# Optimization experiments

Measured on AMD Instinct MI355X. Metric: run time of the kernel, lower is better.

## Reference

```python
import jax, jax.numpy as jnp
import numpy as np

B, T, D, H, E, K, F = 8, 1024, 512, 8, 8, 2, 2048
HD = D // H
EPS = 1e-5


def _layernorm(x, g, b):
    m = jnp.mean(x, axis=-1, keepdims=True)
    v = jnp.mean((x - m) ** 2, axis=-1, keepdims=True)
    return (x - m) * jax.lax.rsqrt(v + EPS) * g + b


def setup_inputs() -> dict:
    key = jax.random.key(0)
    ks = jax.random.split(key, 12)
    s = lambda d: 1.0 / np.sqrt(d)
    return {
        "x": jax.random.normal(ks[0], (B, T, D), jnp.float32),
        "ln1_g": jnp.ones((D,), jnp.float32),
        "ln1_b": jnp.zeros((D,), jnp.float32),
        "ln2_g": jnp.ones((D,), jnp.float32),
        "ln2_b": jnp.zeros((D,), jnp.float32),
        "Wqkv": jax.random.normal(ks[1], (D, 3 * D), jnp.float32) * s(D),
        "bqkv": jnp.zeros((3 * D,), jnp.float32),
        "Wo": jax.random.normal(ks[2], (D, D), jnp.float32) * s(D),
        "bo": jnp.zeros((D,), jnp.float32),
        "Wg": jax.random.normal(ks[3], (D, E), jnp.float32) * s(D),
        "We1": jax.random.normal(ks[4], (E, D, F), jnp.float32) * s(D),
        "be1": jnp.zeros((E, F), jnp.float32),
        "We2": jax.random.normal(ks[5], (E, F, D), jnp.float32) * s(F),
        "be2": jnp.zeros((E, D), jnp.float32),
    }


def _attn(x, Wqkv, bqkv, Wo, bo):
    qkv = x @ Wqkv + bqkv                      # [B,T,3D]
    q, k, v = jnp.split(qkv, 3, axis=-1)
    q = q.reshape(B, T, H, HD)
    k = k.reshape(B, T, H, HD)
    v = v.reshape(B, T, H, HD)
    scores = jnp.einsum("bqhd,bkhd->bhqk", q, k) / np.sqrt(HD)
    causal = jnp.tril(jnp.ones((T, T), bool))
    scores = jnp.where(causal, scores, jnp.finfo(scores.dtype).min)
    p = jax.nn.softmax(scores, axis=-1)
    o = jnp.einsum("bhqk,bkhd->bqhd", p, v).reshape(B, T, D)
    return o @ Wo + bo


def _moe(h, Wg, We1, be1, We2, be2):
    hf = h.reshape(-1, D)                      # [N,D]
    N = hf.shape[0]
    probs = jax.nn.softmax(hf @ Wg, axis=-1)   # [N,E]
    topw, topi = jax.lax.top_k(probs, K)       # [N,K]
    topw = topw / jnp.sum(topw, axis=-1, keepdims=True)
    gates = jnp.zeros((N, E), hf.dtype).at[jnp.arange(N)[:, None], topi].add(topw)
    out = jnp.zeros_like(hf)
    for e in range(E):                         # fixed small expert loop
        hid = jax.nn.gelu(hf @ We1[e] + be1[e])
        out = out + gates[:, e:e + 1] * (hid @ We2[e] + be2[e])
    return out.reshape(h.shape)


def reference(x, ln1_g, ln1_b, ln2_g, ln2_b, Wqkv, bqkv, Wo, bo, Wg, We1, be1, We2, be2):
    # Pipeline chunking over batch is a scheduling detail; math is the plain block.
    h = x + _attn(_layernorm(x, ln1_g, ln1_b), Wqkv, bqkv, Wo, bo)
    return h + _moe(_layernorm(h, ln2_g, ln2_b), Wg, We1, be1, We2, be2)
```

## Files before the change

kernel.cpp:

```cpp
#include <hip/hip_runtime.h>


typedef unsigned short u16;
typedef unsigned int   u32;
typedef unsigned long long u64;
typedef __attribute__((ext_vector_type(8))) short short8;
typedef __attribute__((ext_vector_type(4))) float f32x4;

#define DEV static __device__ __forceinline__

DEV u16 f2bf(float f){
  union { float f; u32 u; } x; x.f = f;
  return (u16)((x.u + 0x7FFFu + ((x.u >> 16) & 1u)) >> 16);
}
DEV float bf2f(u16 b){
  union { u32 u; float f; } x; x.u = ((u32)b) << 16; return x.f;
}
DEV f32x4 mfma16(short8 a, short8 b, f32x4 c){
  return __builtin_amdgcn_mfma_f32_16x16x32_bf16(a, b, c, 0, 0, 0);
}
DEV void g2l16(const void* g, void* l){
  __builtin_amdgcn_global_load_lds((const __attribute__((address_space(1))) u32*)g,
                                   (__attribute__((address_space(3))) u32*)l, 16, 0, 0);
}
DEV void wait_vm0(){ asm volatile("s_waitcnt vmcnt(0)" ::: "memory"); }

__global__ __launch_bounds__(256) void transpose_cvt2(const float* __restrict__ src,
    u16* __restrict__ dh, u16* __restrict__ dl, int R, int C)
{
  __shared__ float tile[32][33];
  const size_t zb = (size_t)blockIdx.z * R * C;
  src += zb; dh += zb; dl += zb;
  const int tx = threadIdx.x, ty = threadIdx.y;
  const int c0 = blockIdx.x * 32, r0 = blockIdx.y * 32;
  #pragma unroll
  for (int i = 0; i < 4; ++i)
    tile[ty + i*8][tx] = src[(size_t)(r0 + ty + i*8) * C + c0 + tx];
  __syncthreads();
  #pragma unroll
  for (int i = 0; i < 4; ++i){
    float v = tile[tx][ty + i*8];
    size_t o = (size_t)(c0 + ty + i*8) * R + r0 + tx;
    u16 hb = f2bf(v);
    dh[o] = hb;
    dl[o] = f2bf(v - bf2f(hb));
  }
}

__global__ __launch_bounds__(256) void transpose_cvt1(const float* __restrict__ src,
    u16* __restrict__ d, int R, int C)
{
  __shared__ float tile[32][33];
  const size_t zb = (size_t)blockIdx.z * R * C;
  src += zb; d += zb;
  const int tx = threadIdx.x, ty = threadIdx.y;
  const int c0 = blockIdx.x * 32, r0 = blockIdx.y * 32;
  #pragma unroll
  for (int i = 0; i < 4; ++i)
    tile[ty + i*8][tx] = src[(size_t)(r0 + ty + i*8) * C + c0 + tx];
  __syncthreads();
  #pragma unroll
  for (int i = 0; i < 4; ++i)
    d[(size_t)(c0 + ty + i*8) * R + r0 + tx] = f2bf(tile[tx][ty + i*8]);
}

__global__ __launch_bounds__(256) void ln1_kernel(const float* __restrict__ x,
    const float* __restrict__ g, const float* __restrict__ b,
    u16* __restrict__ yh, u16* __restrict__ yl)
{
  const int wid = threadIdx.x >> 6, lane = threadIdx.x & 63;
  const int row = blockIdx.x * 4 + wid;
  const float* xr = x + (size_t)row * 512 + lane * 8;
  f32x4 t0 = ((const f32x4*)xr)[0], t1 = ((const f32x4*)xr)[1];
  float v[8];
  #pragma unroll
  for (int j = 0; j < 8; ++j) v[j] = (j < 4) ? t0[j] : t1[j-4];
  float s = 0.f, q = 0.f;
  #pragma unroll
  for (int j = 0; j < 8; ++j){ s += v[j]; q += v[j]*v[j]; }
  #pragma unroll
  for (int o = 32; o; o >>= 1){ s += __shfl_xor(s, o); q += __shfl_xor(q, o); }
  const float mean = s * (1.f/512.f);
  const float var  = q * (1.f/512.f) - mean*mean;
  const float rstd = rsqrtf(var + 1e-5f);
  f32x4 g0 = ((const f32x4*)(g + lane*8))[0], g1 = ((const f32x4*)(g + lane*8))[1];
  f32x4 b0 = ((const f32x4*)(b + lane*8))[0], b1 = ((const f32x4*)(b + lane*8))[1];
  short8 vh, vl;
  #pragma unroll
  for (int j = 0; j < 8; ++j){
    float gg = (j < 4) ? g0[j] : g1[j-4];
    float bb = (j < 4) ? b0[j] : b1[j-4];
    float y = (v[j]-mean)*rstd*gg + bb;
    u16 hb = f2bf(y);
    vh[j] = (short)hb;
    vl[j] = (short)f2bf(y - bf2f(hb));
  }
  ((short8*)(yh + (size_t)row*512 + lane*8))[0] = vh;
  ((short8*)(yl + (size_t)row*512 + lane*8))[0] = vl;
}

template<int MODE>
__global__ __launch_bounds__(256) void gemm_split2(
    const u16* __restrict__ Ah, const u16* __restrict__ Al,
    const u16* __restrict__ Bh, const u16* __restrict__ Bl,
    const float* __restrict__ bias, int K,
    u16* __restrict__ q_h, u16* __restrict__ q_l, u16* __restrict__ q_m,
    u16* __restrict__ k_h, u16* __restrict__ k_l, u16* __restrict__ k_m,
    u16* __restrict__ v_h, u16* __restrict__ v_l,
    const float* __restrict__ xres, float* __restrict__ hout)
{
  __shared__ u16 Ash[2][128*32], Asl[2][128*32], Bsh[2][128*32], Bsl[2][128*32];
  const int tid = threadIdx.x;
  const int wid = tid >> 6, lane = tid & 63;
  const int wr = wid >> 1, wc = wid & 1;
  const int lr = lane & 15, lg = lane >> 4;
  const int m0 = blockIdx.x * 128, n0 = blockIdx.y * 128;

  size_t aoff[2], boff[2];
  u32 ldso[2];
  #pragma unroll
  for (int r = 0; r < 2; ++r){
    int i = r*256 + tid;
    int row = i >> 2, cc = i & 3;
    int scc = cc ^ ((row >> 1) & 3);
    aoff[r] = ((size_t)(m0+row)*K + scc*8) * 2;
    boff[r] = ((size_t)(n0+row)*K + scc*8) * 2;
    ldso[r] = (u32)(r*256 + wid*64) * 8;
  }

  f32x4 acc[4][4];
  #pragma unroll
  for (int a = 0; a < 4; ++a)
    #pragma unroll
    for (int b = 0; b < 4; ++b) acc[a][b] = 0;

  const char* pAh = (const char*)Ah; const char* pAl = (const char*)Al;
  const char* pBh = (const char*)Bh; const char* pBl = (const char*)Bl;

  auto stage = [&](int sb, int ks){
    const size_t kb = (size_t)ks * 64;
    #pragma unroll
    for (int r = 0; r < 2; ++r){
      g2l16(pAh + aoff[r] + kb, &Ash[sb][0] + ldso[r]);
      g2l16(pAl + aoff[r] + kb, &Asl[sb][0] + ldso[r]);
      g2l16(pBh + boff[r] + kb, &Bsh[sb][0] + ldso[r]);
      g2l16(pBl + boff[r] + kb, &Bsl[sb][0] + ldso[r]);
    }
  };

  const int nks = K >> 5;
  stage(0, 0);
  wait_vm0();
  __syncthreads();
  int buf = 0;
  for (int ks = 0; ks < nks; ++ks){
    if (ks + 1 < nks) stage(buf ^ 1, ks + 1);
    short8 ah[4], al[4], bh[4], bl[4];
    #pragma unroll
    for (int mt = 0; mt < 4; ++mt){
      int row = wr*64 + mt*16 + lr;
      int kcs = lg ^ ((row >> 1) & 3);
      int o = row*32 + kcs*8;
      ah[mt] = *(const short8*)(&Ash[buf][0] + o);
      al[mt] = *(const short8*)(&Asl[buf][0] + o);
    }
    #pragma unroll
    for (int nt = 0; nt < 4; ++nt){
      int row = wc*64 + nt*16 + lr;
      int kcs = lg ^ ((row >> 1) & 3);
      int o = row*32 + kcs*8;
      bh[nt] = *(const short8*)(&Bsh[buf][0] + o);
      bl[nt] = *(const short8*)(&Bsl[buf][0] + o);
    }
    __builtin_amdgcn_s_setprio(1);
    #pragma unroll
    for (int mt = 0; mt < 4; ++mt)
      #pragma unroll
      for (int nt = 0; nt < 4; ++nt){
        f32x4 c = acc[mt][nt];
        c = mfma16(ah[mt], bh[nt], c);
        c = mfma16(ah[mt], bl[nt], c);
        c = mfma16(al[mt], bh[nt], c);
        acc[mt][nt] = c;
      }
    __builtin_amdgcn_s_setprio(0);
    wait_vm0();
    __syncthreads();
    buf ^= 1;
  }

  #pragma unroll
  for (int mt = 0; mt < 4; ++mt){
    #pragma unroll
    for (int nt = 0; nt < 4; ++nt){
      const int col = n0 + wc*64 + nt*16 + lr;
      const float bv = bias[col];
      #pragma unroll
      for (int r2 = 0; r2 < 4; ++r2){
        const int row = m0 + wr*64 + mt*16 + 4*lg + r2;
        const float val = acc[mt][nt][r2] + bv;
        if constexpr (MODE == 0){
          const int which = col >> 9, rem = col & 511;
          const int hh = rem >> 6, hd = rem & 63;
          const int b_ = row >> 10, t_ = row & 1023;
          const size_t idx = ((size_t)(b_*8 + hh)*1024 + t_)*64 + hd;
          const u16 hb = f2bf(val);
          if (which == 2){
            v_h[idx] = hb;
            v_l[idx] = f2bf(val - bf2f(hb));
          } else {
            const float r1 = val - bf2f(hb);
            const u16 lb = f2bf(r1);
            const u16 mb = f2bf(r1 - bf2f(lb));
            if (which == 0){ q_h[idx]=hb; q_l[idx]=lb; q_m[idx]=mb; }
            else           { k_h[idx]=hb; k_l[idx]=lb; k_m[idx]=mb; }
          }
        } else {
          const size_t o = (size_t)row*512 + col;
          hout[o] = val + xres[o];
        }
      }
    }
  }
}

__global__ __launch_bounds__(256) void attn_kernel(
    const u16* __restrict__ q_h, const u16* __restrict__ q_l, const u16* __restrict__ q_m,
    const u16* __restrict__ k_h, const u16* __restrict__ k_l, const u16* __restrict__ k_m,
    const u16* __restrict__ v_h, const u16* __restrict__ v_l,
    u16* __restrict__ aoh, u16* __restrict__ aol)
{
  __shared__ u16 Ksh[64*64], Ksl[64*64], Ksm[64*64];
  __shared__ u16 Vth[64*72], Vtl[64*72];
  __shared__ u16 Ph[4*16*72], Pl[4*16*72];
  const int tid = threadIdx.x, wid = tid >> 6, lane = tid & 63;
  const int lr = lane & 15, lg = lane >> 4;
  const int bfl = blockIdx.x;
  const int xcd = bfl & 7, jj_ = bfl >> 3;
  const int bh = xcd * 8 + (jj_ & 7);
  const int qt = 15 - (jj_ >> 3);
  const int q0 = qt * 64;
  const size_t base = (size_t)bh * 1024 * 64;

  short8 qfh[2], qfl[2], qfm[2];
  {
    const int qrow = q0 + wid*16 + lr;
    #pragma unroll
    for (int c = 0; c < 2; ++c){
      const size_t o = base + (size_t)qrow*64 + c*32 + lg*8;
      qfh[c] = *(const short8*)(q_h + o);
      qfl[c] = *(const short8*)(q_l + o);
      qfm[c] = *(const short8*)(q_m + o);
    }
  }
  f32x4 oacc[4];
  float m_r[4], l_r[4];
  #pragma unroll
  for (int nt = 0; nt < 4; ++nt) oacc[nt] = 0;
  #pragma unroll
  for (int r = 0; r < 4; ++r){ m_r[r] = -1e30f; l_r[r] = 0.f; }

  short8 kreg[3][2];
  short8 vreg[2][2];
  const int pp = tid & 31, d0 = (tid >> 5) * 8;

  auto load_tile = [&](int kt){
    #pragma unroll
    for (int r = 0; r < 2; ++r){
      const int i = r*256 + tid;
      const int row = i >> 3, cc = i & 7;
      const int scc = cc ^ (row & 7);
      const size_t go = base + (size_t)(kt*64 + row)*64 + scc*8;
      kreg[0][r] = *(const short8*)(k_h + go);
      kreg[1][r] = *(const short8*)(k_l + go);
      kreg[2][r] = *(const short8*)(k_m + go);
    }
    const size_t g0 = base + (size_t)(kt*64 + 2*pp)*64 + d0;
    vreg[0][0] = *(const short8*)(v_h + g0);
    vreg[0][1] = *(const short8*)(v_h + g0 + 64);
    vreg[1][0] = *(const short8*)(v_l + g0);
    vreg[1][1] = *(const short8*)(v_l + g0 + 64);
  };

  load_tile(0);
  for (int kt = 0; kt <= qt; ++kt){
    if (kt) __syncthreads();
    #pragma unroll
    for (int r = 0; r < 2; ++r){
      const int o = (r*256 + tid) * 8;
      *(short8*)(Ksh + o) = kreg[0][r];
      *(short8*)(Ksl + o) = kreg[1][r];
      *(short8*)(Ksm + o) = kreg[2][r];
    }
    #pragma unroll
    for (int j = 0; j < 8; ++j){
      u32 ph_ = (u32)(u16)vreg[0][0][j] | ((u32)(u16)vreg[0][1][j] << 16);
      u32 pl_ = (u32)(u16)vreg[1][0][j] | ((u32)(u16)vreg[1][1][j] << 16);
      *(u32*)(Vth + (d0+j)*72 + 2*pp) = ph_;
      *(u32*)(Vtl + (d0+j)*72 + 2*pp) = pl_;
    }
    __syncthreads();
    if (kt < qt) load_tile(kt + 1);
    __builtin_amdgcn_sched_barrier(0);

    f32x4 s[4];
    #pragma unroll
    for (int nt = 0; nt < 4; ++nt) s[nt] = 0;
    __builtin_amdgcn_s_setprio(1);
    #pragma unroll
    for (int c = 0; c < 2; ++c){
      #pragma unroll
      for (int nt = 0; nt < 4; ++nt){
        const int row = nt*16 + lr;
        const int kcs = (c*4 + lg) ^ (row & 7);
        const int o = row*64 + kcs*8;
        short8 kh_ = *(const short8*)(Ksh + o);
        short8 kl_ = *(const short8*)(Ksl + o);
        short8 km_ = *(const short8*)(Ksm + o);
        f32x4 cacc = s[nt];
        cacc = mfma16(qfh[c], kh_, cacc);
        cacc = mfma16(qfh[c], kl_, cacc);
        cacc = mfma16(qfl[c], kh_, cacc);
        cacc = mfma16(qfh[c], km_, cacc);
        cacc = mfma16(qfm[c], kh_, cacc);
        cacc = mfma16(qfl[c], kl_, cacc);
        s[nt] = cacc;
      }
    }
    __builtin_amdgcn_s_setprio(0);
    float sc[4][4];
    const bool last = (kt == qt);
    #pragma unroll
    for (int nt = 0; nt < 4; ++nt)
      #pragma unroll
      for (int r = 0; r < 4; ++r){
        float v = s[nt][r] * 0.125f;
        if (last){
          int qa = q0 + wid*16 + 4*lg + r;
          int ka = kt*64 + nt*16 + lr;
          if (ka > qa) v = -1e30f;
        }
        sc[nt][r] = v;
      }
    float pr[4][4];
    #pragma unroll
    for (int r = 0; r < 4; ++r){
      float mx = fmaxf(fmaxf(sc[0][r], sc[1][r]), fmaxf(sc[2][r], sc[3][r]));
      #pragma unroll
      for (int o2 = 8; o2; o2 >>= 1) mx = fmaxf(mx, __shfl_xor(mx, o2));
      const float nm = fmaxf(m_r[r], mx);
      const float al = __expf(m_r[r] - nm);
      float sum = 0.f;
      #pragma unroll
      for (int nt = 0; nt < 4; ++nt){
        float e_ = __expf(sc[nt][r] - nm);
        pr[nt][r] = e_;
        sum += e_;
      }
      #pragma unroll
      for (int o2 = 8; o2; o2 >>= 1) sum += __shfl_xor(sum, o2);
      l_r[r] = l_r[r]*al + sum;
      m_r[r] = nm;
      #pragma unroll
      for (int nt = 0; nt < 4; ++nt) oacc[nt][r] *= al;
    }
    #pragma unroll
    for (int nt = 0; nt < 4; ++nt)
      #pragma unroll
      for (int r = 0; r < 4; ++r){
        const float pv = pr[nt][r];
        const u16 hb = f2bf(pv);
        const u16 lb = f2bf(pv - bf2f(hb));
        const int o = wid*1152 + (4*lg + r)*72 + nt*16 + lr;
        Ph[o] = hb; Pl[o] = lb;
      }
    #pragma unroll
    for (int c = 0; c < 2; ++c){
      const int po = wid*1152 + lr*72 + c*32 + lg*8;
      short8 pah = *(const short8*)(Ph + po);
      short8 pal = *(const short8*)(Pl + po);
      __builtin_amdgcn_s_setprio(1);
      #pragma unroll
      for (int nt = 0; nt < 4; ++nt){
        const int vo = (nt*16 + lr)*72 + c*32 + lg*8;
        short8 vhf = *(const short8*)(Vth + vo);
        short8 vlf = *(const short8*)(Vtl + vo);
        f32x4 cacc = oacc[nt];
        cacc = mfma16(pah, vhf, cacc);
        cacc = mfma16(pah, vlf, cacc);
        cacc = mfma16(pal, vhf, cacc);
        oacc[nt] = cacc;
      }
      __builtin_amdgcn_s_setprio(0);
    }
  }

  const int b_ = bh >> 3, h_ = bh & 7;
  #pragma unroll
  for (int nt = 0; nt < 4; ++nt)
    #pragma unroll
    for (int r = 0; r < 4; ++r){
      const int qa = q0 + wid*16 + 4*lg + r;
      const float val = oacc[nt][r] / l_r[r];
      const size_t o = ((size_t)(b_*1024 + qa))*512 + h_*64 + nt*16 + lr;
      const u16 hb = f2bf(val);
      aoh[o] = hb;
      aol[o] = f2bf(val - bf2f(hb));
    }
}

__global__ __launch_bounds__(256) void ln2_gate_kernel(const float* __restrict__ h,
    const float* __restrict__ g, const float* __restrict__ b,
    const float* __restrict__ Wg, u16* __restrict__ y2,
    int* __restrict__ ge, float* __restrict__ gw)
{
  const int wid = threadIdx.x >> 6, lane = threadIdx.x & 63;
  const int row = blockIdx.x * 4 + wid;
  const float* xr = h + (size_t)row * 512 + lane * 8;
  f32x4 t0 = ((const f32x4*)xr)[0], t1 = ((const f32x4*)xr)[1];
  float v[8];
  #pragma unroll
  for (int j = 0; j < 8; ++j) v[j] = (j < 4) ? t0[j] : t1[j-4];
  float s = 0.f, q = 0.f;
  #pragma unroll
  for (int j = 0; j < 8; ++j){ s += v[j]; q += v[j]*v[j]; }
  #pragma unroll
  for (int o = 32; o; o >>= 1){ s += __shfl_xor(s, o); q += __shfl_xor(q, o); }
  const float mean = s * (1.f/512.f);
  const float var  = q * (1.f/512.f) - mean*mean;
  const float rstd = rsqrtf(var + 1e-5f);
  f32x4 g0 = ((const f32x4*)(g + lane*8))[0], g1 = ((const f32x4*)(g + lane*8))[1];
  f32x4 b0 = ((const f32x4*)(b + lane*8))[0], b1 = ((const f32x4*)(b + lane*8))[1];
  float yv[8];
  short8 yb;
  #pragma unroll
  for (int j = 0; j < 8; ++j){
    float gg = (j < 4) ? g0[j] : g1[j-4];
    float bb = (j < 4) ? b0[j] : b1[j-4];
    yv[j] = (v[j]-mean)*rstd*gg + bb;
    yb[j] = (short)f2bf(yv[j]);
  }
  ((short8*)(y2 + (size_t)row*512 + lane*8))[0] = yb;

  float lgt[8];
  #pragma unroll
  for (int e = 0; e < 8; ++e) lgt[e] = 0.f;
  #pragma unroll
  for (int j = 0; j < 8; ++j){
    const float* wr_ = Wg + (size_t)(lane*8 + j) * 8;
    #pragma unroll
    for (int e = 0; e < 8; ++e) lgt[e] += yv[j] * wr_[e];
  }
  #pragma unroll
  for (int o = 32; o; o >>= 1){
    #pragma unroll
    for (int e = 0; e < 8; ++e) lgt[e] += __shfl_xor(lgt[e], o);
  }
  if (lane == 0){
    int e0 = 0; float l0 = lgt[0];
    #pragma unroll
    for (int e = 1; e < 8; ++e) if (lgt[e] > l0){ l0 = lgt[e]; e0 = e; }
    int e1 = -1; float l1 = -3e38f;
    #pragma unroll
    for (int e = 0; e < 8; ++e) if (e != e0 && lgt[e] > l1){ l1 = lgt[e]; e1 = e; }
    const float t = expf(l1 - l0);
    const float w0 = 1.f / (1.f + t);
    const float w1 = t * w0;
    ge[row*2]   = e0; ge[row*2+1] = e1;
    gw[row*2]   = w0; gw[row*2+1] = w1;
  }
}

__global__ __launch_bounds__(256) void count_kernel(const int* __restrict__ ge,
                                                    int* __restrict__ cnt)
{
  const int i = blockIdx.x * 256 + threadIdx.x;
  const int lane = threadIdx.x & 63;
  const int e = ge[i];
  #pragma unroll
  for (int ex = 0; ex < 8; ++ex){
    u64 m = __ballot(e == ex);
    if (m && lane == (int)(__ffsll((long long)m) - 1))
      atomicAdd(&cnt[ex], __popcll(m));
  }
}

__global__ void offsets_kernel(int* cnt){
  if (threadIdx.x == 0){
    int o = 0, tp = 0;
    for (int e = 0; e < 8; ++e){
      cnt[8+e] = o; cnt[17+e] = o;
      cnt[25+e] = tp;
      o  += cnt[e];
      tp += (cnt[e] + 127) >> 7;
    }
    cnt[16] = o;
    cnt[33] = tp;
  }
}

__global__ __launch_bounds__(256) void scatter_kernel(const int* __restrict__ ge,
    const float* __restrict__ gw, int* __restrict__ cnt,
    int* __restrict__ rdst, float* __restrict__ rw)
{
  const int i = blockIdx.x * 256 + threadIdx.x;
  const int lane = threadIdx.x & 63;
  const int e = ge[i];
  const float w = gw[i];
  const u64 below = ((u64)1 << lane) - 1;
  int pos = -1;
  #pragma unroll
  for (int ex = 0; ex < 8; ++ex){
    u64 m = __ballot(e == ex);
    if (m){
      const int leader = (int)(__ffsll((long long)m) - 1);
      int base = 0;
      if (lane == leader) base = atomicAdd(&cnt[17 + ex], __popcll(m));
      base = __shfl(base, leader);
      if (e == ex) pos = base + __popcll(m & below);
    }
  }
  rdst[pos] = i;
  rw[pos]   = w;
}

template<int MODE, int TN, int BAND_M, int BPX>
__global__ __launch_bounds__(256, 4) void gemm_moe(
    const u16* __restrict__ A, const u16* __restrict__ Bt,
    const float* __restrict__ bias, int N, int K,
    const int* __restrict__ cntblk,
    const int* __restrict__ rdst, const float* __restrict__ rw,
    u16* __restrict__ hid, float* __restrict__ contrib)
{
  __shared__ u16 As[2][128*32], Bs[2][128*32];
  const int fid = blockIdx.x;
  const int xcd = fid & 7;
  const int j   = fid >> 3;
  const int bpb = BAND_M * TN;
  const int bi  = j / bpb;
  const int r_  = j % bpb;
  const int nt_ = r_ / BAND_M;
  const int mi  = r_ % BAND_M;
  const int mt  = (bi * 8 + xcd) * BAND_M + mi;
  if (mt >= cntblk[33]) return;
  int e = 7;
  #pragma unroll
  for (int k = 7; k >= 1; --k) if (mt < cntblk[25 + k]) e = k - 1;
  const int ce = cntblk[e];
  const int eo = cntblk[8 + e];
  const int m0 = (mt - cntblk[25 + e]) * 128;
  const int n0 = nt_ * 128;

  const int tid = threadIdx.x;
  const int wid = tid >> 6, lane = tid & 63;
  const int wr = wid >> 1, wc = wid & 1;
  const int lr = lane & 15, lg = lane >> 4;

  size_t aoff[2], boff[2];
  u32 ldso[2];
  #pragma unroll
  for (int r = 0; r < 2; ++r){
    int i = r*256 + tid;
    int row = i >> 2, cc = i & 3;
    int scc = cc ^ ((row >> 1) & 3);
    int p = eo + m0 + row;
    const int pmax = eo + ce - 1;
    if (p > pmax) p = pmax;
    const int arow = (MODE == 2) ? (rdst[p] >> 1) : p;
    aoff[r] = ((size_t)arow * K + scc*8) * 2;
    boff[r] = (((size_t)e * N + n0 + row) * K + scc*8) * 2;
    ldso[r] = (u32)(r*256 + wid*64) * 8;
  }

  f32x4 acc[4][4];
  #pragma unroll
  for (int a = 0; a < 4; ++a)
    #pragma unroll
    for (int b = 0; b < 4; ++b) acc[a][b] = 0;

  const char* pA = (const char*)A;
  const char* pB = (const char*)Bt;

  auto stage = [&](int sb, int ks){
    const size_t kb = (size_t)ks * 64;
    #pragma unroll
    for (int r = 0; r < 2; ++r){
      g2l16(pA + aoff[r] + kb, &As[sb][0] + ldso[r]);
      g2l16(pB + boff[r] + kb, &Bs[sb][0] + ldso[r]);
    }
  };

  const int nks = K >> 5;
  stage(0, 0);
  wait_vm0();
  __syncthreads();
  int buf = 0;
  for (int ks = 0; ks < nks; ++ks){
    if (ks + 1 < nks) stage(buf ^ 1, ks + 1);
    short8 av[4], bv[4];
    #pragma unroll
    for (int mt2 = 0; mt2 < 4; ++mt2){
      int row = wr*64 + mt2*16 + lr;
      int kcs = lg ^ ((row >> 1) & 3);
      av[mt2] = *(const short8*)(&As[buf][0] + row*32 + kcs*8);
    }
    #pragma unroll
    for (int nt2 = 0; nt2 < 4; ++nt2){
      int row = wc*64 + nt2*16 + lr;
      int kcs = lg ^ ((row >> 1) & 3);
      bv[nt2] = *(const short8*)(&Bs[buf][0] + row*32 + kcs*8);
    }
    __builtin_amdgcn_s_setprio(1);
    #pragma unroll
    for (int mt2 = 0; mt2 < 4; ++mt2)
      #pragma unroll
      for (int nt2 = 0; nt2 < 4; ++nt2)
        acc[mt2][nt2] = mfma16(av[mt2], bv[nt2], acc[mt2][nt2]);
    __builtin_amdgcn_s_setprio(0);
    wait_vm0();
    __syncthreads();
    buf ^= 1;
  }

  const float* bp = bias + (size_t)e * N;
  #pragma unroll
  for (int mt2 = 0; mt2 < 4; ++mt2){
    #pragma unroll
    for (int nt2 = 0; nt2 < 4; ++nt2){
      const int col = n0 + wc*64 + nt2*16 + lr;
      const float bv2 = bp[col];
      #pragma unroll
      for (int r2 = 0; r2 < 4; ++r2){
        const int lrow = wr*64 + mt2*16 + 4*lg + r2;
        if (m0 + lrow < ce){
          const int p = eo + m0 + lrow;
          const float val = acc[mt2][nt2][r2] + bv2;
          if constexpr (MODE == 2){
            const float gx = val;
            const float z2 = 1.5957691216057308f * (gx + 0.044715f*gx*gx*gx);
            const float gl = gx / (1.f + __expf(-z2));
            hid[(size_t)p * N + col] = f2bf(gl);
          } else {
            contrib[(size_t)rdst[p] * N + col] = val * rw[p];
          }
        }
      }
    }
  }
}

__global__ __launch_bounds__(256) void final_kernel(const float* __restrict__ h,
    const float* __restrict__ contrib, float* __restrict__ out)
{
  const int i = blockIdx.x * 256 + threadIdx.x;
  const int row = i >> 7, rem = i & 127;
  const f32x4* c4 = (const f32x4*)contrib;
  f32x4 hv = ((const f32x4*)h)[i];
  f32x4 a = c4[(size_t)(row*2) * 128 + rem];
  f32x4 b = c4[(size_t)(row*2) * 128 + 128 + rem];
  ((f32x4*)out)[i] = hv + a + b;
}

extern "C" void kernel_launch(void* const* d_in, const int* in_sizes, int n_in,
                              void* d_out, int out_size, void* d_ws, size_t ws_size,
                              hipStream_t stream)
{
  (void)in_sizes; (void)n_in; (void)out_size; (void)ws_size;
  const float* x    = (const float*)d_in[0];
  const float* ln1g = (const float*)d_in[1];
  const float* ln1b = (const float*)d_in[2];
  const float* ln2g = (const float*)d_in[3];
  const float* ln2b = (const float*)d_in[4];
  const float* Wqkv = (const float*)d_in[5];
  const float* bqkv = (const float*)d_in[6];
  const float* Wo   = (const float*)d_in[7];
  const float* bo   = (const float*)d_in[8];
  const float* Wg   = (const float*)d_in[9];
  const float* We1  = (const float*)d_in[10];
  const float* be1  = (const float*)d_in[11];
  const float* We2  = (const float*)d_in[12];
  const float* be2  = (const float*)d_in[13];
  float* out = (float*)d_out;

  char* ws = (char*)d_ws;
  size_t off_ = 0;
  auto alloc = [&](size_t bytes)->char*{
    char* p = ws + off_;
    off_ = (off_ + bytes + 255) & ~(size_t)255;
    return p;
  };
  u16* wqkvTh = (u16*)alloc((size_t)1536*512*2);
  u16* wqkvTl = (u16*)alloc((size_t)1536*512*2);
  u16* woTh   = (u16*)alloc((size_t)512*512*2);
  u16* woTl   = (u16*)alloc((size_t)512*512*2);
  u16* we1T   = (u16*)alloc((size_t)8*2048*512*2);
  u16* we2T   = (u16*)alloc((size_t)8*512*2048*2);
  u16* y1h    = (u16*)alloc((size_t)8192*512*2);
  u16* y1l    = (u16*)alloc((size_t)8192*512*2);
  u16* qh_    = (u16*)alloc((size_t)8192*64*8*2);
  u16* ql_    = (u16*)alloc((size_t)8192*64*8*2);
  u16* qm_    = (u16*)alloc((size_t)8192*64*8*2);
  u16* kh_    = (u16*)alloc((size_t)8192*64*8*2);
  u16* kl_    = (u16*)alloc((size_t)8192*64*8*2);
  u16* km_    = (u16*)alloc((size_t)8192*64*8*2);
  u16* vh_    = (u16*)alloc((size_t)8192*64*8*2);
  u16* vl_    = (u16*)alloc((size_t)8192*64*8*2);
  u16* aoh    = (u16*)alloc((size_t)8192*512*2);
  u16* aol    = (u16*)alloc((size_t)8192*512*2);
  float* hbuf = (float*)alloc((size_t)8192*512*4);
  u16* y2     = (u16*)alloc((size_t)8192*512*2);
  int* ge     = (int*)alloc((size_t)8192*2*4);
  float* gw   = (float*)alloc((size_t)8192*2*4);
  int* cnt    = (int*)alloc(256);
  int* rdst   = (int*)alloc((size_t)16384*4);
  float* rw   = (float*)alloc((size_t)16384*4);
  u16* hid    = (u16*)alloc((size_t)16384*2048*2);
  float* contrib = (float*)alloc((size_t)16384*512*4);

  (void)hipMemsetAsync(cnt, 0, 256, stream);

  const dim3 tb(32, 8);
  transpose_cvt2<<<dim3(48, 16, 1), tb, 0, stream>>>(Wqkv, wqkvTh, wqkvTl, 512, 1536);
  transpose_cvt2<<<dim3(16, 16, 1), tb, 0, stream>>>(Wo,   woTh,   woTl,   512, 512);
  transpose_cvt1<<<dim3(64, 16, 8), tb, 0, stream>>>(We1, we1T, 512, 2048);
  transpose_cvt1<<<dim3(16, 64, 8), tb, 0, stream>>>(We2, we2T, 2048, 512);

  ln1_kernel<<<2048, 256, 0, stream>>>(x, ln1g, ln1b, y1h, y1l);

  gemm_split2<0><<<dim3(64, 12), 256, 0, stream>>>(
      y1h, y1l, wqkvTh, wqkvTl, bqkv, 512,
      qh_, ql_, qm_, kh_, kl_, km_, vh_, vl_, nullptr, nullptr);

  attn_kernel<<<dim3(1024), 256, 0, stream>>>(
      qh_, ql_, qm_, kh_, kl_, km_, vh_, vl_, aoh, aol);

  gemm_split2<1><<<dim3(64, 4), 256, 0, stream>>>(
      aoh, aol, woTh, woTl, bo, 512,
      nullptr, nullptr, nullptr, nullptr, nullptr, nullptr, nullptr, nullptr,
      x, hbuf);

  ln2_gate_kernel<<<2048, 256, 0, stream>>>(hbuf, ln2g, ln2b, Wg, y2, ge, gw);
  count_kernel<<<64, 256, 0, stream>>>(ge, cnt);
  offsets_kernel<<<1, 64, 0, stream>>>(cnt);
  scatter_kernel<<<64, 256, 0, stream>>>(ge, gw, cnt, rdst, rw);

  gemm_moe<2, 16, 2, 9><<<dim3(2304), 256, 0, stream>>>(
      y2, we1T, be1, 2048, 512, cnt, rdst, rw, hid, nullptr);
  gemm_moe<3, 4, 2, 9><<<dim3(576), 256, 0, stream>>>(
      hid, we2T, be2, 512, 2048, cnt, rdst, rw, nullptr, contrib);

  final_kernel<<<4096, 256, 0, stream>>>(hbuf, contrib, out);
}
```

Measured before the change: 421.9 us.

## Split-K the MoE down-projection and atomically accumulate into output

```diff
diff --git a/kernel.cpp b/kernel.cpp
--- a/kernel.cpp
+++ b/kernel.cpp
@@ -412,12 +412,14 @@
 __global__ __launch_bounds__(256) void ln2_gate_kernel(const float* __restrict__ h,
     const float* __restrict__ g, const float* __restrict__ b,
     const float* __restrict__ Wg, u16* __restrict__ y2,
-    int* __restrict__ ge, float* __restrict__ gw)
+    int* __restrict__ ge, float* __restrict__ gw, float* __restrict__ outw)
 {
   const int wid = threadIdx.x >> 6, lane = threadIdx.x & 63;
   const int row = blockIdx.x * 4 + wid;
   const float* xr = h + (size_t)row * 512 + lane * 8;
   f32x4 t0 = ((const f32x4*)xr)[0], t1 = ((const f32x4*)xr)[1];
+  ((f32x4*)(outw + (size_t)row * 512 + lane * 8))[0] = t0;
+  ((f32x4*)(outw + (size_t)row * 512 + lane * 8))[1] = t1;
   float v[8];
   #pragma unroll
   for (int j = 0; j < 8; ++j) v[j] = (j < 4) ? t0[j] : t1[j-4];
@@ -524,24 +526,30 @@
   rw[pos]   = w;
 }
 
-template<int MODE, int TN, int BAND_M, int BPX>
+template<int MODE, int TN, int KSPLIT>
 __global__ __launch_bounds__(256, 4) void gemm_moe(
     const u16* __restrict__ A, const u16* __restrict__ Bt,
     const float* __restrict__ bias, int N, int K,
     const int* __restrict__ cntblk,
     const int* __restrict__ rdst, const float* __restrict__ rw,
-    u16* __restrict__ hid, float* __restrict__ contrib)
+    u16* __restrict__ hid, float* __restrict__ outw)
 {
   __shared__ u16 As[2][128*32], Bs[2][128*32];
   const int fid = blockIdx.x;
   const int xcd = fid & 7;
   const int j   = fid >> 3;
-  const int bpb = BAND_M * TN;
+  const int bpb = 2 * TN * KSPLIT;
   const int bi  = j / bpb;
+  const int cntx = (xcd < 4) ? 9 : 8;
+  if (bi >= cntx) return;
+  const int base_b = (xcd < 4) ? 9*xcd : 36 + 8*(xcd - 4);
+  const int band = base_b + bi;
   const int r_  = j % bpb;
-  const int nt_ = r_ / BAND_M;
-  const int mi  = r_ % BAND_M;
-  const int mt  = (bi * 8 + xcd) * BAND_M + mi;
+  const int nt_ = r_ / (2 * KSPLIT);
+  const int rem = r_ % (2 * KSPLIT);
+  const int mi  = rem / KSPLIT;
+  const int kh  = rem % KSPLIT;
+  const int mt  = band * 2 + mi;
   if (mt >= cntblk[33]) return;
   int e = 7;
   #pragma unroll
@@ -550,6 +558,7 @@
   const int eo = cntblk[8 + e];
   const int m0 = (mt - cntblk[25 + e]) * 128;
   const int n0 = nt_ * 128;
+  const int kbase = kh * (K / KSPLIT);
 
   const int tid = threadIdx.x;
   const int wid = tid >> 6, lane = tid & 63;
@@ -567,8 +576,8 @@
     const int pmax = eo + ce - 1;
     if (p > pmax) p = pmax;
     const int arow = (MODE == 2) ? (rdst[p] >> 1) : p;
-    aoff[r] = ((size_t)arow * K + scc*8) * 2;
-    boff[r] = (((size_t)e * N + n0 + row) * K + scc*8) * 2;
+    aoff[r] = ((size_t)arow * K + kbase + scc*8) * 2;
+    boff[r] = (((size_t)e * N + n0 + row) * K + kbase + scc*8) * 2;
     ldso[r] = (u32)(r*256 + wid*64) * 8;
   }
 
@@ -590,7 +599,7 @@
     }
   };
 
-  const int nks = K >> 5;
+  const int nks = (K / KSPLIT) >> 5;
   stage(0, 0);
   wait_vm0();
   __syncthreads();
@@ -628,7 +637,7 @@
     #pragma unroll
     for (int nt2 = 0; nt2 < 4; ++nt2){
       const int col = n0 + wc*64 + nt2*16 + lr;
-      const float bv2 = bp[col];
+      const float bv2 = (kh == 0) ? bp[col] : 0.f;
       #pragma unroll
       for (int r2 = 0; r2 < 4; ++r2){
         const int lrow = wr*64 + mt2*16 + 4*lg + r2;
@@ -641,24 +650,13 @@
             const float gl = gx / (1.f + __expf(-z2));
             hid[(size_t)p * N + col] = f2bf(gl);
           } else {
-            contrib[(size_t)rdst[p] * N + col] = val * rw[p];
+            const int tok = rdst[p] >> 1;
+            atomicAdd(&outw[(size_t)tok * 512 + col], val * rw[p]);
           }
         }
       }
     }
   }
-}
-
-__global__ __launch_bounds__(256) void final_kernel(const float* __restrict__ h,
-    const float* __restrict__ contrib, float* __restrict__ out)
-{
-  const int i = blockIdx.x * 256 + threadIdx.x;
-  const int row = i >> 7, rem = i & 127;
-  const f32x4* c4 = (const f32x4*)contrib;
-  f32x4 hv = ((const f32x4*)h)[i];
-  f32x4 a = c4[(size_t)(row*2) * 128 + rem];
-  f32x4 b = c4[(size_t)(row*2) * 128 + 128 + rem];
-  ((f32x4*)out)[i] = hv + a + b;
 }
 
 extern "C" void kernel_launch(void* const* d_in, const int* in_sizes, int n_in,
@@ -715,7 +713,6 @@
   int* rdst   = (int*)alloc((size_t)16384*4);
   float* rw   = (float*)alloc((size_t)16384*4);
   u16* hid    = (u16*)alloc((size_t)16384*2048*2);
-  float* contrib = (float*)alloc((size_t)16384*512*4);
 
   (void)hipMemsetAsync(cnt, 0, 256, stream);
 
@@ -739,15 +736,13 @@
       nullptr, nullptr, nullptr, nullptr, nullptr, nullptr, nullptr, nullptr,
       x, hbuf);
 
-  ln2_gate_kernel<<<2048, 256, 0, stream>>>(hbuf, ln2g, ln2b, Wg, y2, ge, gw);
+  ln2_gate_kernel<<<2048, 256, 0, stream>>>(hbuf, ln2g, ln2b, Wg, y2, ge, gw, out);
   count_kernel<<<64, 256, 0, stream>>>(ge, cnt);
   offsets_kernel<<<1, 64, 0, stream>>>(cnt);
   scatter_kernel<<<64, 256, 0, stream>>>(ge, gw, cnt, rdst, rw);
 
-  gemm_moe<2, 16, 2, 9><<<dim3(2304), 256, 0, stream>>>(
+  gemm_moe<2, 16, 1><<<dim3(2304), 256, 0, stream>>>(
       y2, we1T, be1, 2048, 512, cnt, rdst, rw, hid, nullptr);
-  gemm_moe<3, 4, 2, 9><<<dim3(576), 256, 0, stream>>>(
-      hid, we2T, be2, 512, 2048, cnt, rdst, rw, nullptr, contrib);
-
-  final_kernel<<<4096, 256, 0, stream>>>(hbuf, contrib, out);
-}
+  gemm_moe<3, 4, 2><<<dim3(1152), 256, 0, stream>>>(
+      hid, we2T, be2, 512, 2048, cnt, rdst, rw, nullptr, out);
+}
```

After: 475.8 us. 12.8% more time.
